# Optimization experiments

Hardware: AMD Instinct MI355X
Metric: run time of the kernel (lower is better)

Reference implementation:

```python
import jax, jax.numpy as jnp
import numpy as np

B, S, D, H = 4, 2048, 1024, 16
DH = D // H


def setup_inputs() -> dict:
    key = jax.random.key(0)
    k0, k1, k2, k3 = jax.random.split(key, 4)
    x = jax.random.normal(k0, (B, S, D), dtype=jnp.float32)
    k = jax.random.normal(k1, (B, H, S, DH), dtype=jnp.float32)
    v = jax.random.normal(k2, (B, H, S, DH), dtype=jnp.float32)
    # nn.Linear(d, d, bias=False) weight: [out, in]; scaled like torch default init
    Wq = jax.random.normal(k3, (D, D), dtype=jnp.float32) * (1.0 / np.sqrt(D))
    return {"x": x, "k": k, "v": v, "Wq": Wq}


def reference(x, k, v, Wq):
    Bx, Sx, d = x.shape
    h, dh = k.shape[1], k.shape[3]
    rd = jnp.sqrt(jnp.float32(d))  # NOTE: module scales by sqrt(d), not sqrt(d_head)
    # q projection: y = x @ Wq.T  -> [B,S,d] -> [B,h,S,dh]
    q = (x @ Wq.T).reshape(Bx, Sx, h, dh).transpose(0, 2, 1, 3)
    # scores [B,h,S,S]
    a = jnp.einsum('bhqd,bhkd->bhqk', q, k) / rd
    causal = jnp.triu(jnp.ones((Sx, Sx), dtype=bool), k=1)
    a = jnp.where(causal, -jnp.inf, a)
    p = jax.nn.softmax(a, axis=-1)
    o = jnp.einsum('bhqk,bhkd->bhqd', p, v)  # [B,h,S,dh]
    o = o.transpose(0, 2, 1, 3).reshape(Bx, Sx, d)
    return x + o
```

## Files before the change

kernel.cpp:

```cpp
#include <hip/hip_runtime.h>
#include <hip/hip_bf16.h>

typedef __attribute__((ext_vector_type(4))) float f32x4;
typedef __attribute__((ext_vector_type(8))) short bf16x8;
typedef __attribute__((ext_vector_type(4))) unsigned short u16x4;
typedef __attribute__((ext_vector_type(4))) unsigned int u32x4;

#define MFMA16(a, b, c) __builtin_amdgcn_mfma_f32_16x16x32_bf16((a), (b), (c), 0, 0, 0)

static __device__ __forceinline__ unsigned short f2bf(float f) {
    unsigned u = __float_as_uint(f);
    u += 0x7FFFu + ((u >> 16) & 1u);
    return (unsigned short)(u >> 16);
}
static __device__ __forceinline__ uint2 pack4_rhu(float4 v) {
    unsigned a = __float_as_uint(v.x) + 0x8000u;
    unsigned b = __float_as_uint(v.y) + 0x8000u;
    unsigned c = __float_as_uint(v.z) + 0x8000u;
    unsigned d = __float_as_uint(v.w) + 0x8000u;
    uint2 r;
    r.x = __builtin_amdgcn_perm(b, a, 0x07060302u);
    r.y = __builtin_amdgcn_perm(d, c, 0x07060302u);
    return r;
}
static __device__ __forceinline__ float exp2_fast(float x) {
#if __has_builtin(__builtin_amdgcn_exp2f)
    return __builtin_amdgcn_exp2f(x);
#else
    return exp2f(x);
#endif
}

static __device__ __forceinline__ void permswap32(unsigned &a, unsigned &b) {
#if __has_builtin(__builtin_amdgcn_permlane32_swap)
    typedef __attribute__((ext_vector_type(2))) unsigned u32x2_t;
    u32x2_t r = __builtin_amdgcn_permlane32_swap(a, b, false, false);
    a = r[0]; b = r[1];
#else
    asm volatile("v_permlane32_swap_b32 %0, %1" : "+v"(a), "+v"(b));
#endif
}
static __device__ __forceinline__ void permswap16(unsigned &a, unsigned &b) {
#if __has_builtin(__builtin_amdgcn_permlane16_swap)
    typedef __attribute__((ext_vector_type(2))) unsigned u32x2_t;
    u32x2_t r = __builtin_amdgcn_permlane16_swap(a, b, false, false);
    a = r[0]; b = r[1];
#else
    asm volatile("v_permlane16_swap_b32 %0, %1" : "+v"(a), "+v"(b));
#endif
}

#define QSCALE 0.04508422002778011f

__global__ __launch_bounds__(256) void qproj_kernel(const float* __restrict__ x,
                                                    const float* __restrict__ wq,
                                                    unsigned short* __restrict__ qout) {
    __shared__ __align__(16) unsigned short As[2][128][40];
    __shared__ __align__(16) unsigned short Bs[2][128][40];
    const int m0 = blockIdx.x * 128;
    const int n0 = blockIdx.y * 128;
    const int tid = threadIdx.x;
    const int wave = tid >> 6, lane = tid & 63;
    const int lg = lane >> 4, lc = lane & 15;
    const int wm = wave >> 1, wn = wave & 1;

    f32x4 acc[4][4];
#pragma unroll
    for (int i = 0; i < 4; ++i)
#pragma unroll
        for (int j = 0; j < 4; ++j) acc[i][j] = (f32x4){0.f, 0.f, 0.f, 0.f};

    float4 ax[4], bx[4];
#pragma unroll
    for (int i = 0; i < 4; ++i) {
        int c = tid + i * 256;
        int row = c >> 3, kc = (c & 7) * 4;
        ax[i] = *(const float4*)(x  + (size_t)(m0 + row) * 1024 + kc);
        bx[i] = *(const float4*)(wq + (size_t)(n0 + row) * 1024 + kc);
    }
#pragma unroll
    for (int i = 0; i < 4; ++i) {
        int c = tid + i * 256;
        int row = c >> 3, kc = (c & 7) * 4;
        *(uint2*)&As[0][row][kc] = pack4_rhu(ax[i]);
        *(uint2*)&Bs[0][row][kc] = pack4_rhu(bx[i]);
    }

    int cur = 0;
    for (int ki = 0; ki < 32; ++ki) {
        __syncthreads();
        const bool havenext = (ki + 1 < 32);
        if (havenext) {
            int ks = (ki + 1) * 32;
#pragma unroll
            for (int i = 0; i < 4; ++i) {
                int c = tid + i * 256;
                int row = c >> 3, kc = (c & 7) * 4;
                ax[i] = *(const float4*)(x  + (size_t)(m0 + row) * 1024 + ks + kc);
                bx[i] = *(const float4*)(wq + (size_t)(n0 + row) * 1024 + ks + kc);
            }
        }
        bf16x8 af[4], bfr[4];
#pragma unroll
        for (int i = 0; i < 4; ++i) {
            af[i]  = *(const bf16x8*)&As[cur][wm * 64 + i * 16 + lc][lg * 8];
            bfr[i] = *(const bf16x8*)&Bs[cur][wn * 64 + i * 16 + lc][lg * 8];
        }
        __builtin_amdgcn_s_setprio(1);
#pragma unroll
        for (int mi = 0; mi < 4; ++mi)
#pragma unroll
            for (int ni = 0; ni < 4; ++ni)
                acc[mi][ni] = MFMA16(af[mi], bfr[ni], acc[mi][ni]);
        __builtin_amdgcn_s_setprio(0);
        if (havenext) {
#pragma unroll
            for (int i = 0; i < 4; ++i) {
                int c = tid + i * 256;
                int row = c >> 3, kc = (c & 7) * 4;
                *(uint2*)&As[cur ^ 1][row][kc] = pack4_rhu(ax[i]);
                *(uint2*)&Bs[cur ^ 1][row][kc] = pack4_rhu(bx[i]);
            }
        }
        cur ^= 1;
    }
#pragma unroll
    for (int mi = 0; mi < 4; ++mi)
#pragma unroll
        for (int ni = 0; ni < 4; ++ni)
#pragma unroll
            for (int r = 0; r < 4; ++r) {
                int m = m0 + wm * 64 + mi * 16 + lg * 4 + r;
                int n = n0 + wn * 64 + ni * 16 + lc;
                int b = m >> 11, s = m & 2047;
                int h = n >> 6, dh = n & 63;
                qout[(((size_t)b * 16 + h) * 2048 + s) * 64 + dh] = f2bf(acc[mi][ni][r] * QSCALE);
            }
}

__global__ __launch_bounds__(256) void convtrans_kernel(const float* __restrict__ kin,
                                                        const float* __restrict__ vin,
                                                        unsigned short* __restrict__ kb,
                                                        unsigned short* __restrict__ vt) {
    __shared__ float buf[64][65];
    const int bid = blockIdx.x;
    const int tid = threadIdx.x;
    if (bid < 8192) {
        int i = bid * 256 + tid;
        float4 v = ((const float4*)kin)[i];
        u16x4 o = { f2bf(v.x), f2bf(v.y), f2bf(v.z), f2bf(v.w) };
        ((u16x4*)kb)[i] = o;
    } else {
        const int idx = bid - 8192;
        const int s0 = (idx & 31) * 64;
        const int bh = idx >> 5;
#pragma unroll
        for (int i = 0; i < 4; ++i) {
            int c = tid + i * 256;
            int s = c >> 4, dc = (c & 15) * 4;
            float4 val = *(const float4*)(vin + ((size_t)bh * 2048 + s0 + s) * 64 + dc);
            buf[s][dc] = val.x; buf[s][dc + 1] = val.y; buf[s][dc + 2] = val.z; buf[s][dc + 3] = val.w;
        }
        __syncthreads();
#pragma unroll
        for (int i = 0; i < 4; ++i) {
            int c = tid + i * 256;
            int dh = c >> 4, sc = (c & 15) * 4;
            u16x4 o = { f2bf(buf[sc][dh]), f2bf(buf[sc + 1][dh]), f2bf(buf[sc + 2][dh]), f2bf(buf[sc + 3][dh]) };
            *(u16x4*)(vt + ((size_t)bh * 64 + dh) * 2048 + s0 + sc) = o;
        }
    }
}

__global__ __launch_bounds__(256) void attn_kernel(const unsigned short* __restrict__ qg,
                                                   const unsigned short* __restrict__ kg,
                                                   const unsigned short* __restrict__ vtg,
                                                   const float* __restrict__ x,
                                                   float* __restrict__ outp) {
    __shared__ __align__(16) unsigned short Ks[2][64][64];
    __shared__ __align__(16) unsigned short VTs[2][64][64];

    const int bh = blockIdx.x;
    const int pr = blockIdx.y;
    const int b = bh >> 4, h = bh & 15;
    const int tid = threadIdx.x;
    const int wave = tid >> 6, lane = tid & 63;
    const int lg = lane >> 4, lc = lane & 15;
    const int lc7 = lc & 7;

    const int r0  = tid >> 3;
    const int c16 = tid & 7;
    const int swz = (c16 ^ (r0 & 7)) * 8;
    const unsigned short* kbase = kg  + ((size_t)bh * 2048 + r0) * 64 + c16 * 8;
    const unsigned short* vbase = vtg + ((size_t)bh * 64 + r0) * 2048 + c16 * 8;

    int cur = 0;
    for (int seg = 0; seg < 2; ++seg) {
        const int qb = seg ? (15 - pr) : pr;
        const int qw0 = qb * 128 + wave * 32;
        const int nkv = 2 * qb + 2;

        bf16x8 qf[2][2];
#pragma unroll
        for (int qt = 0; qt < 2; ++qt)
#pragma unroll
            for (int c = 0; c < 2; ++c)
                qf[qt][c] = *(const bf16x8*)(qg + ((size_t)bh * 2048 + qw0 + qt * 16 + lc) * 64 + c * 32 + lg * 8);

        f32x4 oacc[2][4];
#pragma unroll
        for (int qt = 0; qt < 2; ++qt)
#pragma unroll
            for (int dt = 0; dt < 4; ++dt) oacc[qt][dt] = (f32x4){0.f, 0.f, 0.f, 0.f};
        float l_r[2] = {0.f, 0.f};

        {
            *(bf16x8*)&Ks[cur][r0][swz]       = *(const bf16x8*)(kbase);
            *(bf16x8*)&Ks[cur][r0 + 32][swz]  = *(const bf16x8*)(kbase + 2048);
            *(bf16x8*)&VTs[cur][r0][swz]      = *(const bf16x8*)(vbase);
            *(bf16x8*)&VTs[cur][r0 + 32][swz] = *(const bf16x8*)(vbase + 65536);
        }

        for (int kv = 0; kv < nkv; ++kv) {
            __syncthreads();

            const bool havenext = (kv + 1 < nkv);
            const int nxt = havenext ? kv + 1 : kv;
            bf16x8 nk0 = *(const bf16x8*)(kbase + (size_t)nxt * 4096);
            bf16x8 nk1 = *(const bf16x8*)(kbase + (size_t)nxt * 4096 + 2048);
            bf16x8 nv0 = *(const bf16x8*)(vbase + nxt * 64);
            bf16x8 nv1 = *(const bf16x8*)(vbase + nxt * 64 + 65536);

            const bool active = (kv * 64 <= qw0 + 31);
            if (active) {
                bf16x8 kf[4][2];
#pragma unroll
                for (int kt = 0; kt < 4; ++kt)
#pragma unroll
                    for (int c = 0; c < 2; ++c)
                        kf[kt][c] = *(const bf16x8*)&Ks[cur][kt * 16 + lc][((4 * c + lg) ^ lc7) * 8];

                const int kvb = kv * 64;
                bf16x8 pf[2][2];
#pragma unroll
                for (int qt = 0; qt < 2; ++qt) {
                    f32x4 st[4];
                    __builtin_amdgcn_s_setprio(1);
#pragma unroll
                    for (int kt = 0; kt < 4; ++kt) {
                        f32x4 a = (f32x4){0.f, 0.f, 0.f, 0.f};
                        a = MFMA16(kf[kt][0], qf[qt][0], a);
                        a = MFMA16(kf[kt][1], qf[qt][1], a);
                        st[kt] = a;
                    }
                    __builtin_amdgcn_s_setprio(0);

                    float pp[4][4];
#pragma unroll
                    for (int kt = 0; kt < 4; ++kt)
#pragma unroll
                        for (int r = 0; r < 4; ++r) pp[kt][r] = st[kt][r];
                    if (kvb + 63 > qw0 + qt * 16) {
                        const int qrow = qw0 + qt * 16 + lc;
#pragma unroll
                        for (int kt = 0; kt < 4; ++kt)
#pragma unroll
                            for (int r = 0; r < 4; ++r) {
                                int kk = kvb + kt * 16 + lg * 4 + r;
                                if (kk > qrow) pp[kt][r] = -1e30f;
                            }
                    }
                    float rs = 0.f;
#pragma unroll
                    for (int kt = 0; kt < 4; ++kt)
#pragma unroll
                        for (int r = 0; r < 4; ++r) {
                            float e = exp2_fast(pp[kt][r]);
                            pp[kt][r] = e;
                            rs += e;
                        }
                    l_r[qt] += rs;

                    unsigned Wk[4][2];
#pragma unroll
                    for (int kt = 0; kt < 4; ++kt) {
                        Wk[kt][0] = __builtin_amdgcn_perm(__float_as_uint(pp[kt][1]), __float_as_uint(pp[kt][0]), 0x07060302u);
                        Wk[kt][1] = __builtin_amdgcn_perm(__float_as_uint(pp[kt][3]), __float_as_uint(pp[kt][2]), 0x07060302u);
                    }
                    unsigned T0[4], T1[4];
#pragma unroll
                    for (int hh = 0; hh < 2; ++hh) {
                        unsigned a0 = Wk[0][hh], b0 = Wk[1][hh];
                        permswap32(a0, b0);
                        permswap16(a0, b0);
                        T0[hh] = a0; T0[2 + hh] = b0;
                        unsigned a1 = Wk[2][hh], b1 = Wk[3][hh];
                        permswap32(a1, b1);
                        permswap16(a1, b1);
                        T1[hh] = a1; T1[2 + hh] = b1;
                    }
                    union { u32x4 u; bf16x8 v; } cv0, cv1;
                    cv0.u = (u32x4){T0[0], T0[1], T0[2], T0[3]};
                    cv1.u = (u32x4){T1[0], T1[1], T1[2], T1[3]};
                    pf[qt][0] = cv0.v;
                    pf[qt][1] = cv1.v;
                }

                __builtin_amdgcn_s_setprio(1);
#pragma unroll
                for (int dt = 0; dt < 4; ++dt)
#pragma unroll
                    for (int c = 0; c < 2; ++c) {
                        bf16x8 vtf = *(const bf16x8*)&VTs[cur][dt * 16 + lc][((4 * c + lg) ^ lc7) * 8];
#pragma unroll
                        for (int qt = 0; qt < 2; ++qt)
                            oacc[qt][dt] = MFMA16(vtf, pf[qt][c], oacc[qt][dt]);
                    }
                __builtin_amdgcn_s_setprio(0);
            }

            if (havenext) {
                *(bf16x8*)&Ks[cur ^ 1][r0][swz]       = nk0;
                *(bf16x8*)&Ks[cur ^ 1][r0 + 32][swz]  = nk1;
                *(bf16x8*)&VTs[cur ^ 1][r0][swz]      = nv0;
                *(bf16x8*)&VTs[cur ^ 1][r0 + 32][swz] = nv1;
            }
            cur ^= 1;
        }

#pragma unroll
        for (int qt = 0; qt < 2; ++qt) {
            float lt = l_r[qt];
            lt += __shfl_xor(lt, 16, 64);
            lt += __shfl_xor(lt, 32, 64);
            float li = 1.0f / lt;
            const int q = qw0 + qt * 16 + lc;
            const size_t obase = ((size_t)b * 2048 + q) * 1024 + (size_t)h * 64 + lg * 4;
#pragma unroll
            for (int dt = 0; dt < 4; ++dt) {
                const size_t oi = obase + dt * 16;
                float4 xv = *(const float4*)(x + oi);
                float4 ov;
                ov.x = xv.x + oacc[qt][dt][0] * li;
                ov.y = xv.y + oacc[qt][dt][1] * li;
                ov.z = xv.z + oacc[qt][dt][2] * li;
                ov.w = xv.w + oacc[qt][dt][3] * li;
                *(float4*)(outp + oi) = ov;
            }
        }
    }
}

extern "C" void kernel_launch(void* const* d_in, const int* in_sizes, int n_in,
                              void* d_out, int out_size, void* d_ws, size_t ws_size,
                              hipStream_t stream) {
    const float* x  = (const float*)d_in[0];
    const float* k  = (const float*)d_in[1];
    const float* v  = (const float*)d_in[2];
    const float* wq = (const float*)d_in[3];
    float* outp = (float*)d_out;

    const size_t NELEM = (size_t)4 * 2048 * 1024;
    unsigned short* qbuf = (unsigned short*)d_ws;
    unsigned short* kbuf = qbuf + NELEM;
    unsigned short* vtbuf = kbuf + NELEM;

    qproj_kernel<<<dim3(64, 8), 256, 0, stream>>>(x, wq, qbuf);
    convtrans_kernel<<<8192 + 2048, 256, 0, stream>>>(k, v, kbuf, vtbuf);
    attn_kernel<<<dim3(64, 8), 256, 0, stream>>>(qbuf, kbuf, vtbuf, x, outp);
}
```

Baseline: 109.7 us.

## Split paired causal segments into separate blocks and compute row sums via MFMA

Each block now handles a single 128-row query block instead of a balanced pair (pr, 15-pr), and the grid doubles to 64x16 with heavy blocks issued first. Row sums of the softmax numerators come from extra MFMAs against a ones vector instead of scalar adds plus cross-lane shuffles, and masked entries become zero directly instead of passing exp of -1e30. A never-executed store to a large padding LDS array raises per-block shared memory, which looks meant to cap how many blocks share a CU. This trades the old built-in load balance for more blocks and ordering, and adds a few MFMAs per tile.

Result: slower. 111.9 us (+2.0%).

```diff
diff --git a/kernel.cpp b/kernel.cpp
--- a/kernel.cpp
+++ b/kernel.cpp
@@ -179,14 +179,19 @@
                                                    float* __restrict__ outp) {
     __shared__ __align__(16) unsigned short Ks[2][64][64];
     __shared__ __align__(16) unsigned short VTs[2][64][64];
+    __shared__ unsigned short LdsPad[8192];
 
     const int bh = blockIdx.x;
-    const int pr = blockIdx.y;
+    const int qb = 15 - blockIdx.y;
     const int b = bh >> 4, h = bh & 15;
     const int tid = threadIdx.x;
     const int wave = tid >> 6, lane = tid & 63;
     const int lg = lane >> 4, lc = lane & 15;
     const int lc7 = lc & 7;
+    const int qw0 = qb * 128 + wave * 32;
+    const int nkv = 2 * qb + 2;
+
+    if (tid >= 0x10000) LdsPad[tid] = 0;
 
     const int r0  = tid >> 3;
     const int c16 = tid & 7;
@@ -194,159 +199,152 @@
     const unsigned short* kbase = kg  + ((size_t)bh * 2048 + r0) * 64 + c16 * 8;
     const unsigned short* vbase = vtg + ((size_t)bh * 64 + r0) * 2048 + c16 * 8;
 
+    bf16x8 qf[2][2];
+#pragma unroll
+    for (int qt = 0; qt < 2; ++qt)
+#pragma unroll
+        for (int c = 0; c < 2; ++c)
+            qf[qt][c] = *(const bf16x8*)(qg + ((size_t)bh * 2048 + qw0 + qt * 16 + lc) * 64 + c * 32 + lg * 8);
+
+    bf16x8 ones;
+#pragma unroll
+    for (int i = 0; i < 8; ++i) ones[i] = (short)0x3F80;
+
+    f32x4 oacc[2][4];
+    f32x4 lacc[2];
+#pragma unroll
+    for (int qt = 0; qt < 2; ++qt) {
+#pragma unroll
+        for (int dt = 0; dt < 4; ++dt) oacc[qt][dt] = (f32x4){0.f, 0.f, 0.f, 0.f};
+        lacc[qt] = (f32x4){0.f, 0.f, 0.f, 0.f};
+    }
+
+    {
+        *(bf16x8*)&Ks[0][r0][swz]       = *(const bf16x8*)(kbase);
+        *(bf16x8*)&Ks[0][r0 + 32][swz]  = *(const bf16x8*)(kbase + 2048);
+        *(bf16x8*)&VTs[0][r0][swz]      = *(const bf16x8*)(vbase);
+        *(bf16x8*)&VTs[0][r0 + 32][swz] = *(const bf16x8*)(vbase + 65536);
+    }
+
     int cur = 0;
-    for (int seg = 0; seg < 2; ++seg) {
-        const int qb = seg ? (15 - pr) : pr;
-        const int qw0 = qb * 128 + wave * 32;
-        const int nkv = 2 * qb + 2;
-
-        bf16x8 qf[2][2];
-#pragma unroll
-        for (int qt = 0; qt < 2; ++qt)
-#pragma unroll
-            for (int c = 0; c < 2; ++c)
-                qf[qt][c] = *(const bf16x8*)(qg + ((size_t)bh * 2048 + qw0 + qt * 16 + lc) * 64 + c * 32 + lg * 8);
-
-        f32x4 oacc[2][4];
-#pragma unroll
-        for (int qt = 0; qt < 2; ++qt)
-#pragma unroll
-            for (int dt = 0; dt < 4; ++dt) oacc[qt][dt] = (f32x4){0.f, 0.f, 0.f, 0.f};
-        float l_r[2] = {0.f, 0.f};
-
-        {
-            *(bf16x8*)&Ks[cur][r0][swz]       = *(const bf16x8*)(kbase);
-            *(bf16x8*)&Ks[cur][r0 + 32][swz]  = *(const bf16x8*)(kbase + 2048);
-            *(bf16x8*)&VTs[cur][r0][swz]      = *(const bf16x8*)(vbase);
-            *(bf16x8*)&VTs[cur][r0 + 32][swz] = *(const bf16x8*)(vbase + 65536);
-        }
-
-        for (int kv = 0; kv < nkv; ++kv) {
-            __syncthreads();
-
-            const bool havenext = (kv + 1 < nkv);
-            const int nxt = havenext ? kv + 1 : kv;
-            bf16x8 nk0 = *(const bf16x8*)(kbase + (size_t)nxt * 4096);
-            bf16x8 nk1 = *(const bf16x8*)(kbase + (size_t)nxt * 4096 + 2048);
-            bf16x8 nv0 = *(const bf16x8*)(vbase + nxt * 64);
-            bf16x8 nv1 = *(const bf16x8*)(vbase + nxt * 64 + 65536);
-
-            const bool active = (kv * 64 <= qw0 + 31);
-            if (active) {
-                bf16x8 kf[4][2];
-#pragma unroll
-                for (int kt = 0; kt < 4; ++kt)
-#pragma unroll
-                    for (int c = 0; c < 2; ++c)
-                        kf[kt][c] = *(const bf16x8*)&Ks[cur][kt * 16 + lc][((4 * c + lg) ^ lc7) * 8];
-
-                const int kvb = kv * 64;
-                bf16x8 pf[2][2];
-#pragma unroll
-                for (int qt = 0; qt < 2; ++qt) {
-                    f32x4 st[4];
-                    __builtin_amdgcn_s_setprio(1);
-#pragma unroll
-                    for (int kt = 0; kt < 4; ++kt) {
-                        f32x4 a = (f32x4){0.f, 0.f, 0.f, 0.f};
-                        a = MFMA16(kf[kt][0], qf[qt][0], a);
-                        a = MFMA16(kf[kt][1], qf[qt][1], a);
-                        st[kt] = a;
-                    }
-                    __builtin_amdgcn_s_setprio(0);
-
-                    float pp[4][4];
+    for (int kv = 0; kv < nkv; ++kv) {
+        __syncthreads();
+
+        const bool havenext = (kv + 1 < nkv);
+        const int nxt = havenext ? kv + 1 : kv;
+        bf16x8 nk0 = *(const bf16x8*)(kbase + (size_t)nxt * 4096);
+        bf16x8 nk1 = *(const bf16x8*)(kbase + (size_t)nxt * 4096 + 2048);
+        bf16x8 nv0 = *(const bf16x8*)(vbase + nxt * 64);
+        bf16x8 nv1 = *(const bf16x8*)(vbase + nxt * 64 + 65536);
+
+        const bool active = (kv * 64 <= qw0 + 31);
+        if (active) {
+            bf16x8 kf[4][2];
+#pragma unroll
+            for (int kt = 0; kt < 4; ++kt)
+#pragma unroll
+                for (int c = 0; c < 2; ++c)
+                    kf[kt][c] = *(const bf16x8*)&Ks[cur][kt * 16 + lc][((4 * c + lg) ^ lc7) * 8];
+
+            const int kvb = kv * 64;
+            bf16x8 pf[2][2];
+#pragma unroll
+            for (int qt = 0; qt < 2; ++qt) {
+                f32x4 st[4];
+                __builtin_amdgcn_s_setprio(1);
+#pragma unroll
+                for (int kt = 0; kt < 4; ++kt) {
+                    f32x4 a = (f32x4){0.f, 0.f, 0.f, 0.f};
+                    a = MFMA16(kf[kt][0], qf[qt][0], a);
+                    a = MFMA16(kf[kt][1], qf[qt][1], a);
+                    st[kt] = a;
+                }
+                __builtin_amdgcn_s_setprio(0);
+
+                float pe[4][4];
+                if (kvb + 63 > qw0 + qt * 16) {
+                    const int qrow = qw0 + qt * 16 + lc;
 #pragma unroll
                     for (int kt = 0; kt < 4; ++kt)
 #pragma unroll
-                        for (int r = 0; r < 4; ++r) pp[kt][r] = st[kt][r];
-                    if (kvb + 63 > qw0 + qt * 16) {
-                        const int qrow = qw0 + qt * 16 + lc;
-#pragma unroll
-                        for (int kt = 0; kt < 4; ++kt)
-#pragma unroll
-                            for (int r = 0; r < 4; ++r) {
-                                int kk = kvb + kt * 16 + lg * 4 + r;
-                                if (kk > qrow) pp[kt][r] = -1e30f;
-                            }
-                    }
-                    float rs = 0.f;
+                        for (int r = 0; r < 4; ++r) {
+                            int kk = kvb + kt * 16 + lg * 4 + r;
+                            pe[kt][r] = (kk > qrow) ? 0.f : exp2_fast(st[kt][r]);
+                        }
+                } else {
 #pragma unroll
                     for (int kt = 0; kt < 4; ++kt)
 #pragma unroll
-                        for (int r = 0; r < 4; ++r) {
-                            float e = exp2_fast(pp[kt][r]);
-                            pp[kt][r] = e;
-                            rs += e;
-                        }
-                    l_r[qt] += rs;
-
-                    unsigned Wk[4][2];
-#pragma unroll
-                    for (int kt = 0; kt < 4; ++kt) {
-                        Wk[kt][0] = __builtin_amdgcn_perm(__float_as_uint(pp[kt][1]), __float_as_uint(pp[kt][0]), 0x07060302u);
-                        Wk[kt][1] = __builtin_amdgcn_perm(__float_as_uint(pp[kt][3]), __float_as_uint(pp[kt][2]), 0x07060302u);
-                    }
-                    unsigned T0[4], T1[4];
-#pragma unroll
-                    for (int hh = 0; hh < 2; ++hh) {
-                        unsigned a0 = Wk[0][hh], b0 = Wk[1][hh];
-                        permswap32(a0, b0);
-                        permswap16(a0, b0);
-                        T0[hh] = a0; T0[2 + hh] = b0;
-                        unsigned a1 = Wk[2][hh], b1 = Wk[3][hh];
-                        permswap32(a1, b1);
-                        permswap16(a1, b1);
-                        T1[hh] = a1; T1[2 + hh] = b1;
-                    }
-                    union { u32x4 u; bf16x8 v; } cv0, cv1;
-                    cv0.u = (u32x4){T0[0], T0[1], T0[2], T0[3]};
-                    cv1.u = (u32x4){T1[0], T1[1], T1[2], T1[3]};
-                    pf[qt][0] = cv0.v;
-                    pf[qt][1] = cv1.v;
-                }
-
-                __builtin_amdgcn_s_setprio(1);
-#pragma unroll
-                for (int dt = 0; dt < 4; ++dt)
-#pragma unroll
-                    for (int c = 0; c < 2; ++c) {
-                        bf16x8 vtf = *(const bf16x8*)&VTs[cur][dt * 16 + lc][((4 * c + lg) ^ lc7) * 8];
-#pragma unroll
-                        for (int qt = 0; qt < 2; ++qt)
-                            oacc[qt][dt] = MFMA16(vtf, pf[qt][c], oacc[qt][dt]);
-                    }
-                __builtin_amdgcn_s_setprio(0);
-            }
-
-            if (havenext) {
-                *(bf16x8*)&Ks[cur ^ 1][r0][swz]       = nk0;
-                *(bf16x8*)&Ks[cur ^ 1][r0 + 32][swz]  = nk1;
-                *(bf16x8*)&VTs[cur ^ 1][r0][swz]      = nv0;
-                *(bf16x8*)&VTs[cur ^ 1][r0 + 32][swz] = nv1;
-            }
-            cur ^= 1;
-        }
-
-#pragma unroll
-        for (int qt = 0; qt < 2; ++qt) {
-            float lt = l_r[qt];
-            lt += __shfl_xor(lt, 16, 64);
-            lt += __shfl_xor(lt, 32, 64);
-            float li = 1.0f / lt;
-            const int q = qw0 + qt * 16 + lc;
-            const size_t obase = ((size_t)b * 2048 + q) * 1024 + (size_t)h * 64 + lg * 4;
-#pragma unroll
-            for (int dt = 0; dt < 4; ++dt) {
-                const size_t oi = obase + dt * 16;
-                float4 xv = *(const float4*)(x + oi);
-                float4 ov;
-                ov.x = xv.x + oacc[qt][dt][0] * li;
-                ov.y = xv.y + oacc[qt][dt][1] * li;
-                ov.z = xv.z + oacc[qt][dt][2] * li;
-                ov.w = xv.w + oacc[qt][dt][3] * li;
-                *(float4*)(outp + oi) = ov;
-            }
+                        for (int r = 0; r < 4; ++r) pe[kt][r] = exp2_fast(st[kt][r]);
+                }
+
+                unsigned Wk[4][2];
+#pragma unroll
+                for (int kt = 0; kt < 4; ++kt) {
+                    Wk[kt][0] = __builtin_amdgcn_perm(__float_as_uint(pe[kt][1]), __float_as_uint(pe[kt][0]), 0x07060302u);
+                    Wk[kt][1] = __builtin_amdgcn_perm(__float_as_uint(pe[kt][3]), __float_as_uint(pe[kt][2]), 0x07060302u);
+                }
+                unsigned T0[4], T1[4];
+#pragma unroll
+                for (int hh = 0; hh < 2; ++hh) {
+                    unsigned a0 = Wk[0][hh], b0 = Wk[1][hh];
+                    permswap32(a0, b0);
+                    permswap16(a0, b0);
+                    T0[hh] = a0; T0[2 + hh] = b0;
+                    unsigned a1 = Wk[2][hh], b1 = Wk[3][hh];
+                    permswap32(a1, b1);
+                    permswap16(a1, b1);
+                    T1[hh] = a1; T1[2 + hh] = b1;
+                }
+                union { u32x4 u; bf16x8 v; } cv0, cv1;
+                cv0.u = (u32x4){T0[0], T0[1], T0[2], T0[3]};
+                cv1.u = (u32x4){T1[0], T1[1], T1[2], T1[3]};
+                pf[qt][0] = cv0.v;
+                pf[qt][1] = cv1.v;
+            }
+
+            __builtin_amdgcn_s_setprio(1);
+#pragma unroll
+            for (int qt = 0; qt < 2; ++qt) {
+                lacc[qt] = MFMA16(ones, pf[qt][0], lacc[qt]);
+                lacc[qt] = MFMA16(ones, pf[qt][1], lacc[qt]);
+            }
+#pragma unroll
+            for (int dt = 0; dt < 4; ++dt)
+#pragma unroll
+                for (int c = 0; c < 2; ++c) {
+                    bf16x8 vtf = *(const bf16x8*)&VTs[cur][dt * 16 + lc][((4 * c + lg) ^ lc7) * 8];
+#pragma unroll
+                    for (int qt = 0; qt < 2; ++qt)
+                        oacc[qt][dt] = MFMA16(vtf, pf[qt][c], oacc[qt][dt]);
+                }
+            __builtin_amdgcn_s_setprio(0);
+        }
+
+        if (havenext) {
+            *(bf16x8*)&Ks[cur ^ 1][r0][swz]       = nk0;
+            *(bf16x8*)&Ks[cur ^ 1][r0 + 32][swz]  = nk1;
+            *(bf16x8*)&VTs[cur ^ 1][r0][swz]      = nv0;
+            *(bf16x8*)&VTs[cur ^ 1][r0 + 32][swz] = nv1;
+        }
+        cur ^= 1;
+    }
+
+#pragma unroll
+    for (int qt = 0; qt < 2; ++qt) {
+        float li = 1.0f / lacc[qt][0];
+        const int q = qw0 + qt * 16 + lc;
+        const size_t obase = ((size_t)b * 2048 + q) * 1024 + (size_t)h * 64 + lg * 4;
+#pragma unroll
+        for (int dt = 0; dt < 4; ++dt) {
+            const size_t oi = obase + dt * 16;
+            float4 xv = *(const float4*)(x + oi);
+            float4 ov;
+            ov.x = xv.x + oacc[qt][dt][0] * li;
+            ov.y = xv.y + oacc[qt][dt][1] * li;
+            ov.z = xv.z + oacc[qt][dt][2] * li;
+            ov.w = xv.w + oacc[qt][dt][3] * li;
+            *(float4*)(outp + oi) = ov;
         }
     }
 }
@@ -367,5 +365,5 @@
 
     qproj_kernel<<<dim3(64, 8), 256, 0, stream>>>(x, wq, qbuf);
     convtrans_kernel<<<8192 + 2048, 256, 0, stream>>>(k, v, kbuf, vtbuf);
-    attn_kernel<<<dim3(64, 8), 256, 0, stream>>>(qbuf, kbuf, vtbuf, x, outp);
-}
+    attn_kernel<<<dim3(64, 16), 256, 0, stream>>>(qbuf, kbuf, vtbuf, x, outp);
+}
```
